# Kernel optimization log

Hardware: AMD Instinct MI355X
Metric: run time of the kernel (lower is better)

Reference implementation:

```python
import jax, jax.numpy as jnp
import numpy as np

B, H, S, DK, DV = 2, 48, 2048, 128, 128
EPS = 1e-6

def _l2norm(x):
    n = jnp.linalg.norm(x, axis=-1, keepdims=True)
    return x / jnp.maximum(n, EPS)

def setup_inputs() -> dict:
    root = jax.random.key(0)
    k0, k1, k2, k3, k4 = jax.random.split(root, 5)
    query = jax.random.normal(k0, (B, H, S, DK), jnp.float32)
    key = jax.random.normal(k1, (B, H, S, DK), jnp.float32)
    value = jax.random.normal(k2, (B, H, S, DV), jnp.float32)
    # g is a per-token log decay: negative, in (-0.5, 0)
    g = -0.5 * jax.random.uniform(k3, (B, H, S), jnp.float32)
    # beta is a sigmoid-like mixing gate in (0, 1)
    beta = jax.random.uniform(k4, (B, H, S), jnp.float32)
    return {"query": query, "key": key, "value": value, "g": g, "beta": beta}

def reference(query, key, value, g, beta):
    """Gated delta-rule linear-attention recurrence.

    state_t = state_{t-1} * exp(g_t)
    delta_t = (v_t - k_t^T state_t) * beta_t
    state_t = state_t + k_t delta_t^T
    out_t   = q_t^T state_t
    with q, k L2-normalized and q scaled by 1/sqrt(dk).
    Returns (output [B,H,S,DV], final_state [B,H,DK,DV]).
    """
    dk = query.shape[-1]
    scale = 1.0 / np.sqrt(dk).astype(np.float32)
    q = _l2norm(query) * scale
    k = _l2norm(key)
    # move seq axis to front for scan: (S, B, H, d)
    qs = jnp.moveaxis(q, 2, 0)
    ks = jnp.moveaxis(k, 2, 0)
    vs = jnp.moveaxis(value, 2, 0)
    gs = jnp.moveaxis(g, 2, 0)
    bs = jnp.moveaxis(beta, 2, 0)

    def step(state, xs):
        q_t, k_t, v_t, g_t, b_t = xs
        state = state * jnp.exp(g_t)[..., None, None]          # [B,H,DK,DV]
        kv_mem = jnp.einsum('bhk,bhkv->bhv', k_t, state)       # read
        delta = (v_t - kv_mem) * b_t[..., None]                # beta-scaled delta
        state = state + jnp.einsum('bhk,bhv->bhkv', k_t, delta)
        out = jnp.einsum('bhk,bhkv->bhv', q_t, state)
        return state, out

    init = jnp.zeros((query.shape[0], query.shape[1], dk, value.shape[-1]), query.dtype)
    final_state, outs = jax.lax.scan(step, init, (qs, ks, vs, gs, bs))
    output = jnp.moveaxis(outs, 0, 2)  # [B,H,S,DV]
    return output, final_state
```

## Files before the change

### kernel.cpp

```cpp
#include <hip/hip_runtime.h>

typedef __attribute__((ext_vector_type(8)))  short short8;
typedef __attribute__((ext_vector_type(4)))  float f32x4;
typedef __attribute__((ext_vector_type(16))) float f32x16;
typedef __attribute__((ext_vector_type(4)))  unsigned short ushort4v;

#define NH   96
#define SEQL 2048
#define DD   128
#define CC   64
#define NCH  32
#define SK   136
#define S64  72
#define SLOT 4608

__device__ __forceinline__ unsigned short f2bf(float f){
  union { float f; unsigned u; } v; v.f = f;
  unsigned r = v.u + 0x7FFFu + ((v.u >> 16) & 1u);
  return (unsigned short)(r >> 16);
}
__device__ __forceinline__ float bf2f(unsigned short u){
  union { unsigned u; float f; } v; v.u = ((unsigned)u) << 16; return v.f;
}
__device__ __forceinline__ short8 frg(const unsigned short* b, int stride, int row0, int kt, int lane){
  return *(const short8*)&b[(row0 + (lane & 31)) * stride + (kt << 4) + ((lane >> 5) << 3)];
}
__device__ __forceinline__ short8 ifrag(int n0, int kt, int lane){
  const int idx = n0 + (lane & 31) - (kt << 4) - ((lane >> 5) << 3);
  short8 v;
  #pragma unroll
  for (int e = 0; e < 8; ++e) v[e] = (short)((e == idx) ? 0x3F80 : 0);
  return v;
}
#define MM32(A,B,C) __builtin_amdgcn_mfma_f32_32x32x16_bf16(A,B,C,0,0,0)
__device__ __forceinline__ f32x16 z16(){
  return (f32x16){0.f,0.f,0.f,0.f,0.f,0.f,0.f,0.f,0.f,0.f,0.f,0.f,0.f,0.f,0.f,0.f};
}
template<int KTN>
__device__ __forceinline__ f32x16 gemm32(const unsigned short* A, int sa, int m0,
                                         const unsigned short* B, int sb, int n0,
                                         f32x16 acc, int lane){
  #pragma unroll
  for (int kt = 0; kt < KTN; ++kt)
    acc = MM32(frg(A, sa, m0, kt, lane), frg(B, sb, n0, kt, lane), acc);
  return acc;
}
__device__ __forceinline__ void stq(unsigned short* buf, int stride, int n0, int m0, int lane, f32x16 v){
  const int nn = n0 + (lane & 31), hh = (lane >> 5) << 2;
  #pragma unroll
  for (int q = 0; q < 4; ++q) {
    ushort4v pv;
    #pragma unroll
    for (int s = 0; s < 4; ++s) pv[s] = f2bf(v[4*q + s]);
    *(ushort4v*)&buf[nn * stride + m0 + 8*q + hh] = pv;
  }
}
__device__ __forceinline__ void stqf(float* buf, int stride, int n0, int m0, int lane, f32x16 v){
  const int nn = n0 + (lane & 31), hh = (lane >> 5) << 2;
  #pragma unroll
  for (int q = 0; q < 4; ++q) {
    f32x4 pv;
    #pragma unroll
    for (int s = 0; s < 4; ++s) pv[s] = v[4*q + s];
    *(f32x4*)&buf[nn * stride + m0 + 8*q + hh] = pv;
  }
}
__device__ __forceinline__ f32x16 ldq(const unsigned short* buf, int stride, int n0, int m0, int lane){
  f32x16 a;
  const int nn = n0 + (lane & 31), hh = (lane >> 5) << 2;
  #pragma unroll
  for (int q = 0; q < 4; ++q) {
    ushort4v pv = *(const ushort4v*)&buf[nn * stride + m0 + 8*q + hh];
    #pragma unroll
    for (int s = 0; s < 4; ++s) a[4*q + s] = bf2f(pv[s]);
  }
  return a;
}
__device__ __forceinline__ f32x16 pinit(const unsigned short* lo, const unsigned short* hi,
                                        int nt, int m0, int lane){
  const unsigned short* base = (nt ? hi : lo) + (lane & 31) * S64;
  const int hh = (lane >> 5) << 2;
  f32x16 p;
  #pragma unroll
  for (int q = 0; q < 4; ++q) {
    ushort4v t = *(const ushort4v*)&base[m0 + 8*q + hh];
    #pragma unroll
    for (int s = 0; s < 4; ++s) p[4*q + s] = bf2f(t[s]);
  }
  return p;
}
#define BAR() do { asm volatile("s_waitcnt lgkmcnt(0)" ::: "memory"); __builtin_amdgcn_s_barrier(); } while(0)

#define REC  36864
#define QOFF 0
#define WOFF 8192
#define UOFF 16384
#define KOFF 24576
#define MOFF 32768

#define AOF 0
#define BOF 9216
#define XS0 17920
#define XS1 22528
#define XS2 27136
#define XS3 31744
#define MRO 36352

__global__ __launch_bounds__(256, 2)
void gdn_prep(const float* __restrict__ Qg, const float* __restrict__ Kg,
              const float* __restrict__ Vg, const float* __restrict__ Gg,
              const float* __restrict__ Bg,
              unsigned short* __restrict__ wsp, float* __restrict__ wcs)
{
  __shared__ unsigned short a[40448];
  __shared__ float s_swv[64], s_swiv[64], s_sbe[64];

  const int tid = threadIdx.x, w = tid >> 6, lane = tid & 63;
  const int mt = w >> 1, nt = w & 1;
  const int hc = blockIdx.x, head = hc >> 5, c = hc & 31;
  const int t0 = c * CC;
  const size_t rb = (size_t)head * SEQL * DD + (size_t)t0 * DD;
  const float* kp = Kg + rb;
  const float* qp = Qg + rb;
  const float* vp = Vg + rb;
  const float* gp = Gg + (size_t)head * SEQL + t0;
  const float* bp = Bg + (size_t)head * SEQL + t0;
  unsigned short* rec = wsp + (size_t)hc * REC;

  const int lrow = tid >> 2, cb = (tid & 3) * 32;
  const int cq16 = (tid & 3) * 16;

  f32x4 kr[8], qr[8], vr[8];
  #pragma unroll
  for (int i = 0; i < 8; ++i) {
    kr[i] = *(const f32x4*)(kp + (size_t)lrow * DD + cb + 4*i);
    qr[i] = *(const f32x4*)(qp + (size_t)lrow * DD + cb + 4*i);
    vr[i] = *(const f32x4*)(vp + (size_t)lrow * DD + cb + 4*i);
  }
  float gl = gp[lane], bl = bp[lane];
  float sc = gl;
  #pragma unroll
  for (int d = 1; d < 64; d <<= 1) { float t = __shfl_up(sc, d); if (lane >= d) sc += t; }
  float wv = __expf(sc);
  if (w == 0) { s_swv[lane] = wv; s_swiv[lane] = __expf(-sc); s_sbe[lane] = bl; }
  float ssk = 0.f, ssq = 0.f;
  #pragma unroll
  for (int i = 0; i < 8; ++i) {
    ssk += kr[i][0]*kr[i][0] + kr[i][1]*kr[i][1] + kr[i][2]*kr[i][2] + kr[i][3]*kr[i][3];
    ssq += qr[i][0]*qr[i][0] + qr[i][1]*qr[i][1] + qr[i][2]*qr[i][2] + qr[i][3]*qr[i][3];
  }
  ssk += __shfl_xor(ssk, 1); ssk += __shfl_xor(ssk, 2);
  ssq += __shfl_xor(ssq, 1); ssq += __shfl_xor(ssq, 2);
  const float ik = 1.f / fmaxf(sqrtf(ssk), 1e-6f);
  const float wl = __shfl(wv, lrow);
  const float iq = 0.08838834764831845f / fmaxf(sqrtf(ssq), 1e-6f) * wl;
  #pragma unroll
  for (int i = 0; i < 8; ++i) {
    ushort4v pk, pq;
    #pragma unroll
    for (int r = 0; r < 4; ++r) { pk[r] = f2bf(kr[i][r]*ik); pq[r] = f2bf(qr[i][r]*iq); }
    *(ushort4v*)&a[AOF + lrow*SK + cb + 4*i] = pk;
    *(ushort4v*)&a[BOF + lrow*SK + cb + 4*i] = pq;
    *(ushort4v*)(rec + QOFF + lrow*DD + cb + 4*i) = pq;
  }
  BAR();

  {
    f32x16 ckk = gemm32<8>(a+AOF, SK, 32*mt, a+AOF, SK, 32*nt, z16(), lane);
    f32x16 ckq = gemm32<8>(a+AOF, SK, 32*mt, a+BOF, SK, 32*nt, z16(), lane);
    const int nn = 32*nt + (lane & 31), hh = (lane >> 5) << 2;
    const float ben = s_sbe[nn], wvn = s_swv[nn], sin = s_swiv[nn];
    #pragma unroll
    for (int q = 0; q < 4; ++q) {
      ushort4v xT, xR, mv;
      #pragma unroll
      for (int si = 0; si < 4; ++si) {
        const int r = 4*q + si, mm = 32*mt + 8*q + hh + si;
        const float svm = s_swv[mm], sim = s_swiv[mm], bem = s_sbe[mm];
        xT[si] = (mm > nn) ? f2bf(bem*svm*sin*ckk[r]) : 0;
        xR[si] = (nn > mm) ? f2bf(ben*wvn*sim*ckk[r]) : 0;
        mv[si] = (mm <= nn) ? f2bf(ckq[r]*sim) : 0;
      }
      const int off = nn*S64 + 32*mt + 8*q + hh;
      *(ushort4v*)&a[XS1 + off] = xT;
      *(ushort4v*)&a[XS0 + off] = xR;
      const int blk = (32*mt + 8*q + hh) >> 2;
      *(ushort4v*)&a[MRO + nn*64 + ((blk ^ (nn & 15)) << 2)] = mv;
    }
  }
  BAR();

  {
    f32x16 c1 = gemm32<4>(a+XS0, S64, 32*mt, a+XS1, S64, 32*nt, z16(), lane);
    f32x16 c2 = gemm32<4>(a+XS1, S64, 32*mt, a+XS0, S64, 32*nt, z16(), lane);
    stq(a+XS3, S64, 32*nt, 32*mt, lane, c1);
    stq(a+XS2, S64, 32*nt, 32*mt, lane, c2);
    unsigned short* p0 = a + ((lrow < 32) ? BOF : BOF+2304) + (lrow & 31)*S64;
    const unsigned short* x0 = a + XS0 + lrow*S64;
    #pragma unroll
    for (int jj = 0; jj < 2; ++jj) {
      short8 xv = *(const short8*)&x0[cq16 + 8*jj];
      short8 ov;
      #pragma unroll
      for (int e = 0; e < 8; ++e) {
        const int col = cq16 + 8*jj + e;
        ov[e] = (short)f2bf(((col == lrow) ? 1.f : 0.f) - bf2f((unsigned short)xv[e]));
      }
      *(short8*)&p0[cq16 + 8*jj] = ov;
    }
    #pragma unroll
    for (int b = 0; b < 4; ++b) {
      const int blk = (cq16 >> 2) + b, bh = blk ^ (lrow & 15);
      unsigned long long v = *(const unsigned long long*)&a[MRO + lrow*64 + bh*4];
      *(unsigned long long*)(rec + MOFF + lrow*64 + cq16 + b*4) = v;
    }
  }
  BAR();

  #pragma unroll
  for (int lev = 0; lev < 2; ++lev) {
    const int sr = (lev & 1) ? XS0 : XS2;
    const int st = (lev & 1) ? XS1 : XS3;
    const int dr = (lev & 1) ? XS2 : XS0;
    const int dt = (lev & 1) ? XS3 : XS1;
    const int pp = lev & 1;
    unsigned short* plo_s = a + (pp ? BOF+SLOT : BOF);
    unsigned short* phi_s = a + (pp ? MRO : BOF+2304);
    unsigned short* plo_d = a + (pp ? BOF : BOF+SLOT);
    unsigned short* phi_d = a + (pp ? BOF+2304 : MRO);
    f32x16 c1 = gemm32<4>(a+sr, S64, 32*mt, a+st, S64, 32*nt, z16(), lane);
    if (lev < 1) {
      f32x16 c2 = gemm32<4>(a+st, S64, 32*mt, a+sr, S64, 32*nt, z16(), lane);
      stq(a+dt, S64, 32*nt, 32*mt, lane, c1);
      stq(a+dr, S64, 32*nt, 32*mt, lane, c2);
    } else {
      stq(a+XS2, S64, 32*nt, 32*mt, lane, c1);
    }
    f32x16 p = pinit(plo_s, phi_s, nt, 32*mt, lane);
    p = gemm32<4>(a+st, S64, 32*mt, (nt ? phi_s : plo_s), S64, 0, p, lane);
    stq((nt ? phi_d : plo_d), S64, 0, 32*mt, lane, p);
    BAR();
  }

  {
    f32x16 p = pinit(a+BOF, a+BOF+2304, nt, 32*mt, lane);
    p = gemm32<4>(a+XS2, S64, 32*mt, (nt ? a+BOF+2304 : a+BOF), S64, 0, p, lane);
    stq((nt ? a+MRO : a+BOF+SLOT), S64, 0, 32*mt, lane, p);
    #pragma unroll
    for (int i = 0; i < 8; ++i)
      #pragma unroll
      for (int r = 0; r < 4; ++r)
        a[XS0 + (cb + 4*i + r)*S64 + lrow] = f2bf(vr[i][r]);
  }
  BAR();

  {
    unsigned short* trow  = a + ((lrow < 32) ? BOF+SLOT : MRO) + (lrow & 31)*S64;
    unsigned short* t3row = a + ((lrow < 32) ? BOF : BOF+2304) + (lrow & 31)*S64;
    #pragma unroll
    for (int jj = 0; jj < 2; ++jj) {
      short8 tv = *(const short8*)&trow[cq16 + 8*jj];
      short8 o2, o3;
      #pragma unroll
      for (int e = 0; e < 8; ++e) {
        const int j = cq16 + 8*jj + e;
        const float t = bf2f((unsigned short)tv[e]);
        o2[e] = (short)f2bf(-t * s_sbe[j] * s_swv[j]);
        o3[e] = (short)f2bf( t * s_sbe[j]);
      }
      *(short8*)&trow[cq16 + 8*jj]  = o2;
      *(short8*)&t3row[cq16 + 8*jj] = o3;
    }
    #pragma unroll
    for (int j = 0; j < 2; ++j) {
      f32x16 ckt = z16();
      #pragma unroll
      for (int kk = 0; kk < 2; ++kk) {
        const int kt = 2*w + kk;
        ckt = MM32(frg(a+AOF, SK, 32*j, kt, lane), ifrag(32*w, kt, lane), ckt);
      }
      stq(a+XS2, S64, 32*w, 32*j, lane, ckt);
    }
  }
  BAR();

  f32x16 uacc[2];
  {
    #pragma unroll
    for (int j = 0; j < 2; ++j) {
      f32x16 cw = gemm32<4>(a+XS2, S64, 32*w, (j ? a+MRO : a+BOF+SLOT), S64, 0, z16(), lane);
      stq(a+AOF, SK, 32*j, 32*w, lane, cw);
      uacc[j] = gemm32<4>((j ? a+BOF+2304 : a+BOF), S64, 0, a+XS0, S64, 32*w, z16(), lane);
    }
  }
  BAR();

  {
    const int r2 = tid >> 2, seg = (tid & 3) * 32;
    #pragma unroll
    for (int j2 = 0; j2 < 4; ++j2) {
      short8 v8 = *(const short8*)&a[AOF + r2*SK + seg + 8*j2];
      *(short8*)(rec + WOFF + r2*128 + seg + 8*j2) = v8;
    }
    const int r = tid >> 1, half = (tid & 1) * 32;
    const float wc = s_swv[63];
    #pragma unroll
    for (int j2 = 0; j2 < 4; ++j2) {
      short8 kv = *(const short8*)&a[XS2 + r*S64 + half + 8*j2];
      short8 o;
      #pragma unroll
      for (int e = 0; e < 8; ++e) {
        const int tok = half + 8*j2 + e;
        o[e] = (short)f2bf(bf2f((unsigned short)kv[e]) * wc * s_swiv[tok]);
      }
      *(short8*)(rec + KOFF + r*64 + half + 8*j2) = o;
    }
    unsigned short* uq = a + ((w == 0) ? BOF : (w == 1) ? BOF+2304 : (w == 2) ? BOF+SLOT : MRO);
    stq(uq, S64, 0, 0, lane, uacc[0]);
    stq(uq, S64, 0, 32, lane, uacc[1]);
    if (tid == 0) wcs[hc] = wc;
  }
  BAR();

  {
    const int r = tid >> 1, half = (tid & 1) * 32;
    const unsigned short* qb = a + ((r < 32) ? BOF : (r < 64) ? BOF+2304 : (r < 96) ? BOF+SLOT : MRO);
    #pragma unroll
    for (int j2 = 0; j2 < 4; ++j2) {
      short8 v8 = *(const short8*)&qb[(r & 31)*S64 + half + 8*j2];
      *(short8*)(rec + UOFF + r*64 + half + 8*j2) = v8;
    }
  }
}

#define SU   72
#define OW   0
#define OK0  8704
#define OK1  17920
#define OU   27136
#define OM0  31744
#define OM1  36352
#define OS0T 40960
#define ODT  49664

__global__ __launch_bounds__(512, 1)
void gdn_scan(const unsigned short* __restrict__ wsp, const float* __restrict__ wcs,
              float* __restrict__ Out, float* __restrict__ FS)
{
  __shared__ unsigned short a[54272];
  __shared__ float s_ob[64*68];

  const int tid = threadIdx.x, w = tid >> 6, lane = tid & 63;
  const int head = blockIdx.x % NH, vh = blockIdx.x / NH;
  const unsigned short* recs = wsp + (size_t)head * NCH * REC;
  float* op = Out + (size_t)head * SEQL * DD + vh * 64;

  const int mtS = w >> 1, ntS = w & 1;
  const int mt4 = (w & 3) >> 1, nt4 = w & 1;

  f32x16 s = z16(), oqr = z16();

  const int wr = tid >> 3, wc16 = (tid & 7) * 16;
  const int kr = tid >> 2, kc16 = (tid & 3) * 16;
  const int ur = tid >> 3, uc8 = (tid & 7) * 8;

  short8 stW0, stW1, stK0, stK1, stU, stM, qb[8];
  float wc_cur = 0.f, wcn = 0.f;

  auto issue = [&](int c){
    const unsigned short* rec = recs + (size_t)c * REC;
    stW0 = *(const short8*)(rec + WOFF + wr*128 + wc16);
    stW1 = *(const short8*)(rec + WOFF + wr*128 + wc16 + 8);
    stK0 = *(const short8*)(rec + KOFF + kr*64 + kc16);
    stK1 = *(const short8*)(rec + KOFF + kr*64 + kc16 + 8);
    stU  = *(const short8*)(rec + UOFF + (vh*64 + ur)*64 + uc8);
    stM  = *(const short8*)(rec + MOFF + ur*64 + uc8);
    if (w >= 4) {
      #pragma unroll
      for (int kt = 0; kt < 8; ++kt)
        qb[kt] = *(const short8*)(rec + QOFF + (32*nt4 + (lane & 31))*DD + kt*16 + ((lane >> 5) << 3));
    }
    wcn = wcs[head*NCH + c];
  };
  auto dswrite = [&](int par){
    *(short8*)&a[OW + wr*SK + wc16]     = stW0;
    *(short8*)&a[OW + wr*SK + wc16 + 8] = stW1;
    unsigned short* bk = a + (par ? OK1 : OK0);
    *(short8*)&bk[kr*SU + kc16]     = stK0;
    *(short8*)&bk[kr*SU + kc16 + 8] = stK1;
    *(short8*)&a[OU + ur*SU + uc8] = stU;
    unsigned short* bm = a + (par ? OM1 : OM0);
    *(short8*)&bm[ur*SU + uc8] = stM;
  };

  issue(0);
  wc_cur = wcn;
  dswrite(0);
  stq(a+OS0T, SK, 32*ntS, 32*mtS, lane, s);
  BAR();

  for (int c = 0; c < NCH; ++c) {
    const int cur = c & 1;

    if (c > 0) {
      const int row = tid >> 3, c8 = (tid & 7) * 8;
      f32x4 v0 = *(const f32x4*)&s_ob[row*68 + c8];
      f32x4 v1 = *(const f32x4*)&s_ob[row*68 + c8 + 4];
      float* dst = op + (size_t)((c-1)*CC + row) * DD + c8;
      *(f32x4*)dst = v0;
      *(f32x4*)(dst + 4) = v1;
    }
    if (w < 4) {
      f32x16 d = gemm32<8>(a+OW, SK, 32*mt4, a+OS0T, SK, 32*nt4, z16(), lane);
      const int nn = 32*nt4 + (lane & 31), hh = (lane >> 5) << 2;
      #pragma unroll
      for (int q = 0; q < 4; ++q) {
        ushort4v u4 = *(const ushort4v*)&a[OU + nn*SU + 32*mt4 + 8*q + hh];
        ushort4v pt;
        #pragma unroll
        for (int si = 0; si < 4; ++si) pt[si] = f2bf(d[4*q+si] + bf2f(u4[si]));
        *(ushort4v*)&a[ODT + nn*SU + 32*mt4 + 8*q + hh] = pt;
      }
    } else {
      f32x16 o = z16();
      #pragma unroll
      for (int kt = 0; kt < 8; ++kt)
        o = MM32(frg(a+OS0T, SK, 32*mt4, kt, lane), qb[kt], o);
      oqr = o;
    }
    if (c < NCH-1) issue(c+1);
    BAR();

    {
      f32x16 sa;
      #pragma unroll
      for (int r = 0; r < 16; ++r) sa[r] = s[r] * wc_cur;
      s = gemm32<4>(a + (cur ? OK1 : OK0), SU, 32*mtS, a+ODT, SU, 32*ntS, sa, lane);
    }
    if (w >= 4) {
      f32x16 o = gemm32<4>(a+ODT, SU, 32*mt4, a + (cur ? OM1 : OM0), SU, 32*nt4, oqr, lane);
      stqf(s_ob, 68, 32*nt4, 32*mt4, lane, o);
    }
    stq(a+OS0T, SK, 32*ntS, 32*mtS, lane, s);
    if (c < NCH-1) { dswrite(cur ^ 1); wc_cur = wcn; }
    BAR();
  }

  {
    const int row = tid >> 3, c8 = (tid & 7) * 8;
    f32x4 v0 = *(const f32x4*)&s_ob[row*68 + c8];
    f32x4 v1 = *(const f32x4*)&s_ob[row*68 + c8 + 4];
    float* dst = op + (size_t)((NCH-1)*CC + row) * DD + c8;
    *(f32x4*)dst = v0;
    *(f32x4*)(dst + 4) = v1;
  }
  {
    float* fsp = FS + (size_t)head * DD * DD + vh * 64;
    const int nn = 32*ntS + (lane & 31), hh = (lane >> 5) << 2;
    #pragma unroll
    for (int q = 0; q < 4; ++q)
      #pragma unroll
      for (int si = 0; si < 4; ++si)
        fsp[(size_t)(32*mtS + 8*q + hh + si) * DD + nn] = s[4*q + si];
  }
}

__global__ __launch_bounds__(512, 1)
void gdn_chunk2(const float* __restrict__ Qg, const float* __restrict__ Kg,
                const float* __restrict__ Vg, const float* __restrict__ Gg,
                const float* __restrict__ Bg,
                float* __restrict__ Out, float* __restrict__ FS)
{
  __shared__ __align__(16) unsigned short sKc[64*SK];
  __shared__ __align__(16) unsigned short sQc[64*SK];
  __shared__ __align__(16) unsigned short sS0T[64*SK];
  __shared__ __align__(16) unsigned short sVc[64*S64];
  __shared__ __align__(16) unsigned short sVT[64*S64];
  __shared__ __align__(16) unsigned short sM[64*S64];
  __shared__ __align__(16) unsigned short sAr[8*SLOT];
  __shared__ float sbe2[2][64], swv2[2][64], swiv2[2][64];

  const int tid  = threadIdx.x;
  const int w    = tid >> 6;
  const int lane = tid & 63;
  const int half = w >> 2;
  const int j    = w & 3;
  const int mt   = j >> 1, nt = j & 1;
  const int mtS  = w >> 1, ntS = w & 1;
  const int mtK  = w >> 2, ntK = w & 3;
  const int head = blockIdx.x % NH;
  const int vh   = blockIdx.x / NH;

  const size_t rb = (size_t)head * SEQL * DD;
  const float* qp = Qg + rb;
  const float* kp = Kg + rb;
  const float* vp = Vg + rb + vh * 64;
  const float* gp = Gg + (size_t)head * SEQL;
  const float* bp = Bg + (size_t)head * SEQL;
  float* op  = Out + rb + vh * 64;
  float* fsp = FS + (size_t)head * DD * DD + vh * 64;

  const int lrow = tid >> 3;
  const int c16  = (tid & 7) * 16;
  const int c8   = (tid & 7) * 8;

  unsigned short* const sl0 = sAr + 0*SLOT;
  unsigned short* const sl1 = sAr + 1*SLOT;
  unsigned short* const sl2 = sAr + 2*SLOT;
  unsigned short* const sl3 = sAr + 3*SLOT;
  unsigned short* const sl4 = sAr + 4*SLOT;
  unsigned short* const sl5 = sAr + 5*SLOT;
  unsigned short* const sl6 = sAr + 6*SLOT;
  unsigned short* const sl7 = sAr + 7*SLOT;

  f32x16 s = z16(), oacc = z16();
  f32x4 kr[4], qr[4], vr[2]; float gr = 0.f, br = 0.f;

  auto prefetch = [&](int t0p){
    const float* kb = kp + (size_t)(t0p + lrow) * DD + c16;
    const float* qb = qp + (size_t)(t0p + lrow) * DD + c16;
    const float* vb = vp + (size_t)(t0p + lrow) * DD + c8;
    #pragma unroll
    for (int i = 0; i < 4; ++i) { kr[i] = *(const f32x4*)(kb + 4*i); qr[i] = *(const f32x4*)(qb + 4*i); }
    #pragma unroll
    for (int i = 0; i < 2; ++i) vr[i] = *(const f32x4*)(vb + 4*i);
    if (w == 7) { gr = gp[t0p + lane]; br = bp[t0p + lane]; }
  };
  auto scan_to = [&](int p){
    if (w == 7) {
      float sc = gr;
      #pragma unroll
      for (int d = 1; d < 64; d <<= 1) { float t = __shfl_up(sc, d); if (lane >= d) sc += t; }
      swv2[p][lane]  = __expf(sc);
      swiv2[p][lane] = __expf(-sc);
      sbe2[p][lane]  = br;
    }
  };

  prefetch(0);
  scan_to(0);
  BAR();

  for (int tc = 0; tc < NCH; ++tc) {
    const int t0 = tc * CC;
    const int cur = tc & 1, nxt = cur ^ 1;
    {
      float ssk = 0.f, ssq = 0.f;
      #pragma unroll
      for (int i = 0; i < 4; ++i) {
        ssk += kr[i][0]*kr[i][0] + kr[i][1]*kr[i][1] + kr[i][2]*kr[i][2] + kr[i][3]*kr[i][3];
        ssq += qr[i][0]*qr[i][0] + qr[i][1]*qr[i][1] + qr[i][2]*qr[i][2] + qr[i][3]*qr[i][3];
      }
      ssk += __shfl_xor(ssk, 1); ssk += __shfl_xor(ssk, 2); ssk += __shfl_xor(ssk, 4);
      ssq += __shfl_xor(ssq, 1); ssq += __shfl_xor(ssq, 2); ssq += __shfl_xor(ssq, 4);
      const float ik = 1.f / fmaxf(sqrtf(ssk), 1e-6f);
      const float iq = 0.08838834764831845f / fmaxf(sqrtf(ssq), 1e-6f) * swv2[cur][lrow];
      #pragma unroll
      for (int i = 0; i < 4; ++i) {
        ushort4v pk, pq;
        #pragma unroll
        for (int r = 0; r < 4; ++r) { pk[r] = f2bf(kr[i][r] * ik); pq[r] = f2bf(qr[i][r] * iq); }
        *(ushort4v*)&sKc[lrow*SK + c16 + 4*i] = pk;
        *(ushort4v*)&sQc[lrow*SK + c16 + 4*i] = pq;
      }
      #pragma unroll
      for (int i = 0; i < 2; ++i) {
        ushort4v pv;
        #pragma unroll
        for (int r = 0; r < 4; ++r) pv[r] = f2bf(vr[i][r]);
        *(ushort4v*)&sVc[lrow*S64 + c8 + 4*i] = pv;
      }
    }
    stq(sS0T, SK, 32*ntS, 32*mtS, lane, s);
    prefetch(tc < NCH-1 ? (tc+1)*CC : t0);
    BAR();

    if (half == 0) {
      f32x16 aa = gemm32<8>(sKc, SK, 32*mt, sKc, SK, 32*nt, z16(), lane);
      const int nn = 32*nt + (lane & 31), hh = (lane >> 5) << 2;
      #pragma unroll
      for (int q = 0; q < 4; ++q) {
        ushort4v pR, pL, pPT, pP;
        #pragma unroll
        for (int si = 0; si < 4; ++si) {
          const int r = 4*q + si, mm = 32*mt + 8*q + hh + si;
          const float S = aa[r];
          const float av  = (mm > nn) ? sbe2[cur][mm]*swv2[cur][mm]*swiv2[cur][nn]*S : 0.f;
          const float atr = (nn > mm) ? sbe2[cur][nn]*swv2[cur][nn]*swiv2[cur][mm]*S : 0.f;
          pR[si]  = f2bf(av);
          pL[si]  = f2bf(atr);
          pPT[si] = f2bf(((mm==nn)?1.f:0.f) - av);
          pP[si]  = f2bf(((mm==nn)?1.f:0.f) - atr);
        }
        const int off = nn*S64 + 32*mt + 8*q + hh;
        *(ushort4v*)&sl1[off] = pR;
        *(ushort4v*)&sl0[off] = pL;
        *(ushort4v*)&sl5[off] = pPT;
        *(ushort4v*)&sl4[off] = pP;
      }
    } else {
      f32x16 aa = gemm32<8>(sKc, SK, 32*mt, sQc, SK, 32*nt, z16(), lane);
      const int nn = 32*nt + (lane & 31), hh = (lane >> 5) << 2;
      #pragma unroll
      for (int q = 0; q < 4; ++q) {
        ushort4v pv;
        #pragma unroll
        for (int si = 0; si < 4; ++si) {
          const int r = 4*q + si, mm = 32*mt + 8*q + hh + si;
          pv[si] = f2bf((mm <= nn) ? aa[r]*swiv2[cur][mm] : 0.f);
        }
        *(ushort4v*)&sM[nn*S64 + 32*mt + 8*q + hh] = pv;
      }
    }
    BAR();

    if (half == 0) {
      f32x16 aa = gemm32<4>(sl0, S64, 32*mt, sl1, S64, 32*nt, z16(), lane);
      stq(sl3, S64, 32*nt, 32*mt, lane, aa);
      f32x16 bb = z16();
      #pragma unroll
      for (int kk = 0; kk < 2; ++kk) {
        const int kt = 2*nt + kk;
        bb = MM32(frg(sVc, S64, 32*mt, kt, lane), ifrag(32*nt, kt, lane), bb);
      }
      stq(sVT, S64, 32*nt, 32*mt, lane, bb);
    } else {
      f32x16 aa = gemm32<4>(sl1, S64, 32*mt, sl0, S64, 32*nt, z16(), lane);
      stq(sl2, S64, 32*nt, 32*mt, lane, aa);
      oacc = gemm32<8>(sQc, SK, 32*mt, sS0T, SK, 32*nt, z16(), lane);
    }
    BAR();

    {
      unsigned short* const inL[3]   = { sl2, sl0, sl2 };
      unsigned short* const inR[3]   = { sl3, sl1, sl3 };
      unsigned short* const outL[3]  = { sl0, sl2, sl0 };
      unsigned short* const outR[3]  = { sl1, sl3, sl1 };
      unsigned short* const inP[3]   = { sl4, sl7, sl5 };
      unsigned short* const inPT[3]  = { sl5, sl6, sl4 };
      unsigned short* const outP[3]  = { sl7, sl5, sl7 };
      unsigned short* const outPT[3] = { sl6, sl4, sl6 };
      #pragma unroll
      for (int lev = 0; lev < 3; ++lev) {
        if (half == 0) {
          f32x16 aa = gemm32<4>(inL[lev], S64, 32*mt, inR[lev], S64, 32*nt, z16(), lane);
          stq(outR[lev], S64, 32*nt, 32*mt, lane, aa);
          f32x16 p = ldq(inPT[lev], S64, 32*nt, 32*mt, lane);
          p = gemm32<4>(inP[lev], S64, 32*mt, inR[lev], S64, 32*nt, p, lane);
          stq(outPT[lev], S64, 32*nt, 32*mt, lane, p);
        } else {
          f32x16 aa = gemm32<4>(inR[lev], S64, 32*mt, inL[lev], S64, 32*nt, z16(), lane);
          stq(outL[lev], S64, 32*nt, 32*mt, lane, aa);
          f32x16 p = ldq(inP[lev], S64, 32*nt, 32*mt, lane);
          p = gemm32<4>(inR[lev], S64, 32*mt, inP[lev], S64, 32*nt, p, lane);
          stq(outP[lev], S64, 32*nt, 32*mt, lane, p);
        }
        BAR();
      }
    }

    if (half == 0) {
      f32x16 aa = gemm32<4>(sl0, S64, 32*mt, sl1, S64, 32*nt, z16(), lane);
      stq(sl2, S64, 32*nt, 32*mt, lane, aa);
    } else {
      f32x16 p = ldq(sl7, S64, 32*nt, 32*mt, lane);
      p = gemm32<4>(sl1, S64, 32*mt, sl7, S64, 32*nt, p, lane);
      stq(sl4, S64, 32*nt, 32*mt, lane, p);
    }
    BAR();

    if (half == 0) {
      f32x16 p = ldq(sl4, S64, 32*nt, 32*mt, lane);
      p = gemm32<4>(sl2, S64, 32*mt, sl4, S64, 32*nt, p, lane);
      const int nn = 32*nt + (lane & 31), hh = (lane >> 5) << 2;
      #pragma unroll
      for (int q = 0; q < 4; ++q) {
        ushort4v p2, p3;
        #pragma unroll
        for (int si = 0; si < 4; ++si) {
          const int r = 4*q + si, mm = 32*mt + 8*q + hh + si;
          const float t = p[r];
          p2[si] = f2bf(-t * sbe2[cur][mm] * swv2[cur][mm]);
          p3[si] = f2bf( t * sbe2[cur][mm]);
        }
        const int off = nn*S64 + 32*mt + 8*q + hh;
        *(ushort4v*)&sl1[off] = p2;
        *(ushort4v*)&sl5[off] = p3;
      }
    } else {
      f32x16 zz = gemm32<8>(sKc, SK, 32*mt, sS0T, SK, 32*nt, z16(), lane);
      stq(sl0, S64, 32*nt, 32*mt, lane, zz);
    }
    {
      f32x16 aa = z16();
      #pragma unroll
      for (int kk = 0; kk < 2; ++kk) {
        const int kt = 2*ntK + kk;
        aa = MM32(frg(sKc, SK, 32*mtK, kt, lane), ifrag(32*ntK, kt, lane), aa);
      }
      stq(sl6, S64, 32*ntK, 32*mtK, lane, aa);
    }
    BAR();

    if (half == 0) {
      f32x16 d = gemm32<4>(sl5, S64, 32*mt, sVT, S64, 32*nt, z16(), lane);
      d = gemm32<4>(sl1, S64, 32*mt, sl0, S64, 32*nt, d, lane);
      const int nn = 32*nt + (lane & 31), hh = (lane >> 5) << 2;
      const float w63 = swv2[cur][63];
      #pragma unroll
      for (int q = 0; q < 4; ++q) {
        ushort4v pt, ps;
        #pragma unroll
        for (int si = 0; si < 4; ++si) {
          const int r = 4*q + si, mm = 32*mt + 8*q + hh + si;
          pt[si] = f2bf(d[r]);
          ps[si] = f2bf(d[r] * w63 * swiv2[cur][mm]);
        }
        const int off = nn*S64 + 32*mt + 8*q + hh;
        *(ushort4v*)&sl3[off] = pt;
        *(ushort4v*)&sl2[off] = ps;
      }
    }
    scan_to(nxt);
    {
      const float w63 = swv2[cur][63];
      #pragma unroll
      for (int r = 0; r < 16; ++r) s[r] *= w63;
    }
    BAR();

    s = gemm32<4>(sl6, S64, 32*mtS, sl2, S64, 32*ntS, s, lane);
    if (half == 1) {
      f32x16 o = oacc;
      o = gemm32<4>(sM, S64, 32*mt, sl3, S64, 32*nt, o, lane);
      const int nn = 32*nt + (lane & 31), hh = (lane >> 5) << 2;
      #pragma unroll
      for (int q = 0; q < 4; ++q)
        #pragma unroll
        for (int si = 0; si < 4; ++si)
          op[(size_t)(t0 + 32*mt + 8*q + hh + si) * DD + nn] = o[4*q + si];
    }
    BAR();
  }

  {
    const int nn = 32*ntS + (lane & 31), hh = (lane >> 5) << 2;
    #pragma unroll
    for (int q = 0; q < 4; ++q)
      #pragma unroll
      for (int si = 0; si < 4; ++si)
        fsp[(size_t)(32*mtS + 8*q + hh + si) * DD + nn] = s[4*q + si];
  }
}

extern "C" void kernel_launch(void* const* d_in, const int* in_sizes, int n_in,
                              void* d_out, int out_size, void* d_ws, size_t ws_size,
                              hipStream_t stream) {
  const float* Q = (const float*)d_in[0];
  const float* K = (const float*)d_in[1];
  const float* V = (const float*)d_in[2];
  const float* G = (const float*)d_in[3];
  const float* B = (const float*)d_in[4];
  float* Out = (float*)d_out;
  float* FS  = Out + (size_t)NH * SEQL * DD;

  const size_t WS_NEED = (size_t)NH * NCH * REC * 2 + (size_t)NH * NCH * 4;
  if (ws_size >= WS_NEED) {
    unsigned short* wsp = (unsigned short*)d_ws;
    float* wcs = (float*)(wsp + (size_t)NH * NCH * REC);
    hipLaunchKernelGGL(gdn_prep, dim3(NH*NCH), dim3(256), 0, stream, Q, K, V, G, B, wsp, wcs);
    hipLaunchKernelGGL(gdn_scan, dim3(NH*2), dim3(512), 0, stream, wsp, wcs, Out, FS);
  } else {
    hipLaunchKernelGGL(gdn_chunk2, dim3(NH*2), dim3(512), 0, stream, Q, K, V, G, B, Out, FS);
  }
}
```

Baseline: 254.8 us.

## Double-buffer scan state and operands to drop one barrier per chunk

The scan loop now double-buffers the W, U and state tiles in LDS. All eight waves compute the delta-term product redundantly instead of splitting it, so the mid-chunk barrier is removed and each chunk needs only one barrier. Output is written straight from registers to global memory rather than staged through an LDS buffer. The precompute kernel also writes W, U, M and K records directly from registers, removing an extra LDS staging pass and two barriers. In exchange LDS use and redundant MFMA work per chunk go up, and the direct global output stores are strided.

```diff
diff --git a/kernel.cpp b/kernel.cpp
--- a/kernel.cpp
+++ b/kernel.cpp
@@ -53,16 +53,6 @@
     #pragma unroll
     for (int s = 0; s < 4; ++s) pv[s] = f2bf(v[4*q + s]);
     *(ushort4v*)&buf[nn * stride + m0 + 8*q + hh] = pv;
-  }
-}
-__device__ __forceinline__ void stqf(float* buf, int stride, int n0, int m0, int lane, f32x16 v){
-  const int nn = n0 + (lane & 31), hh = (lane >> 5) << 2;
-  #pragma unroll
-  for (int q = 0; q < 4; ++q) {
-    f32x4 pv;
-    #pragma unroll
-    for (int s = 0; s < 4; ++s) pv[s] = v[4*q + s];
-    *(f32x4*)&buf[nn * stride + m0 + 8*q + hh] = pv;
   }
 }
 __device__ __forceinline__ f32x16 ldq(const unsigned short* buf, int stride, int n0, int m0, int lane){
@@ -184,8 +174,7 @@
       const int off = nn*S64 + 32*mt + 8*q + hh;
       *(ushort4v*)&a[XS1 + off] = xT;
       *(ushort4v*)&a[XS0 + off] = xR;
-      const int blk = (32*mt + 8*q + hh) >> 2;
-      *(ushort4v*)&a[MRO + nn*64 + ((blk ^ (nn & 15)) << 2)] = mv;
+      *(ushort4v*)(rec + MOFF + nn*64 + 32*mt + 8*q + hh) = mv;
     }
   }
   BAR();
@@ -207,12 +196,6 @@
         ov[e] = (short)f2bf(((col == lrow) ? 1.f : 0.f) - bf2f((unsigned short)xv[e]));
       }
       *(short8*)&p0[cq16 + 8*jj] = ov;
-    }
-    #pragma unroll
-    for (int b = 0; b < 4; ++b) {
-      const int blk = (cq16 >> 2) + b, bh = blk ^ (lrow & 15);
-      unsigned long long v = *(const unsigned long long*)&a[MRO + lrow*64 + bh*4];
-      *(unsigned long long*)(rec + MOFF + lrow*64 + cq16 + b*4) = v;
     }
   }
   BAR();
@@ -271,6 +254,7 @@
       *(short8*)&trow[cq16 + 8*jj]  = o2;
       *(short8*)&t3row[cq16 + 8*jj] = o3;
     }
+    const float wcv = s_swv[63];
     #pragma unroll
     for (int j = 0; j < 2; ++j) {
       f32x16 ckt = z16();
@@ -280,92 +264,82 @@
         ckt = MM32(frg(a+AOF, SK, 32*j, kt, lane), ifrag(32*w, kt, lane), ckt);
       }
       stq(a+XS2, S64, 32*w, 32*j, lane, ckt);
+      const int nn = 32*w + (lane & 31), hh = (lane >> 5) << 2;
+      #pragma unroll
+      for (int q = 0; q < 4; ++q) {
+        ushort4v o;
+        #pragma unroll
+        for (int si = 0; si < 4; ++si) {
+          const int tok = 32*j + 8*q + hh + si;
+          o[si] = f2bf(ckt[4*q+si] * wcv * s_swiv[tok]);
+        }
+        *(ushort4v*)(rec + KOFF + nn*64 + 32*j + 8*q + hh) = o;
+      }
     }
   }
   BAR();
 
-  f32x16 uacc[2];
   {
+    const int nn = lane & 31, hh = (lane >> 5) << 2;
     #pragma unroll
     for (int j = 0; j < 2; ++j) {
       f32x16 cw = gemm32<4>(a+XS2, S64, 32*w, (j ? a+MRO : a+BOF+SLOT), S64, 0, z16(), lane);
-      stq(a+AOF, SK, 32*j, 32*w, lane, cw);
-      uacc[j] = gemm32<4>((j ? a+BOF+2304 : a+BOF), S64, 0, a+XS0, S64, 32*w, z16(), lane);
-    }
-  }
-  BAR();
-
-  {
-    const int r2 = tid >> 2, seg = (tid & 3) * 32;
-    #pragma unroll
-    for (int j2 = 0; j2 < 4; ++j2) {
-      short8 v8 = *(const short8*)&a[AOF + r2*SK + seg + 8*j2];
-      *(short8*)(rec + WOFF + r2*128 + seg + 8*j2) = v8;
-    }
-    const int r = tid >> 1, half = (tid & 1) * 32;
-    const float wc = s_swv[63];
-    #pragma unroll
-    for (int j2 = 0; j2 < 4; ++j2) {
-      short8 kv = *(const short8*)&a[XS2 + r*S64 + half + 8*j2];
-      short8 o;
-      #pragma unroll
-      for (int e = 0; e < 8; ++e) {
-        const int tok = half + 8*j2 + e;
-        o[e] = (short)f2bf(bf2f((unsigned short)kv[e]) * wc * s_swiv[tok]);
-      }
-      *(short8*)(rec + KOFF + r*64 + half + 8*j2) = o;
-    }
-    unsigned short* uq = a + ((w == 0) ? BOF : (w == 1) ? BOF+2304 : (w == 2) ? BOF+SLOT : MRO);
-    stq(uq, S64, 0, 0, lane, uacc[0]);
-    stq(uq, S64, 0, 32, lane, uacc[1]);
-    if (tid == 0) wcs[hc] = wc;
-  }
-  BAR();
-
-  {
-    const int r = tid >> 1, half = (tid & 1) * 32;
-    const unsigned short* qb = a + ((r < 32) ? BOF : (r < 64) ? BOF+2304 : (r < 96) ? BOF+SLOT : MRO);
-    #pragma unroll
-    for (int j2 = 0; j2 < 4; ++j2) {
-      short8 v8 = *(const short8*)&qb[(r & 31)*S64 + half + 8*j2];
-      *(short8*)(rec + UOFF + r*64 + half + 8*j2) = v8;
-    }
+      #pragma unroll
+      for (int q = 0; q < 4; ++q) {
+        ushort4v pw;
+        #pragma unroll
+        for (int si = 0; si < 4; ++si) pw[si] = f2bf(cw[4*q+si]);
+        *(ushort4v*)(rec + WOFF + (32*j + nn)*128 + 32*w + 8*q + hh) = pw;
+      }
+      f32x16 cu = gemm32<4>((j ? a+BOF+2304 : a+BOF), S64, 0, a+XS0, S64, 32*w, z16(), lane);
+      #pragma unroll
+      for (int q = 0; q < 4; ++q) {
+        ushort4v pu;
+        #pragma unroll
+        for (int si = 0; si < 4; ++si) pu[si] = f2bf(cu[4*q+si]);
+        *(ushort4v*)(rec + UOFF + (32*w + nn)*64 + 32*j + 8*q + hh) = pu;
+      }
+    }
+    if (tid == 0) wcs[hc] = s_swv[63];
   }
 }
 
 #define SU   72
-#define OW   0
-#define OK0  8704
-#define OK1  17920
-#define OU   27136
-#define OM0  31744
-#define OM1  36352
-#define OS0T 40960
-#define ODT  49664
+#define OW0  0
+#define OW1  8704
+#define OK0  17408
+#define OK1  26624
+#define OU0  35840
+#define OU1  40448
+#define OM0  45056
+#define OM1  49664
+#define OS0  54272
+#define OS1  62976
+#define ODT  71680
 
 __global__ __launch_bounds__(512, 1)
 void gdn_scan(const unsigned short* __restrict__ wsp, const float* __restrict__ wcs,
               float* __restrict__ Out, float* __restrict__ FS)
 {
-  __shared__ unsigned short a[54272];
-  __shared__ float s_ob[64*68];
+  __shared__ unsigned short a[76288];
 
   const int tid = threadIdx.x, w = tid >> 6, lane = tid & 63;
   const int head = blockIdx.x % NH, vh = blockIdx.x / NH;
   const unsigned short* recs = wsp + (size_t)head * NCH * REC;
+  const float* wcsh = wcs + head * NCH;
   float* op = Out + (size_t)head * SEQL * DD + vh * 64;
 
   const int mtS = w >> 1, ntS = w & 1;
-  const int mt4 = (w & 3) >> 1, nt4 = w & 1;
-
-  f32x16 s = z16(), oqr = z16();
+  const bool outw = (w < 4);
+
+  f32x16 s = z16();
 
   const int wr = tid >> 3, wc16 = (tid & 7) * 16;
   const int kr = tid >> 2, kc16 = (tid & 3) * 16;
   const int ur = tid >> 3, uc8 = (tid & 7) * 8;
 
   short8 stW0, stW1, stK0, stK1, stU, stM, qb[8];
-  float wc_cur = 0.f, wcn = 0.f;
+  float wcn = 0.f;
 
   auto issue = [&](int c){
     const unsigned short* rec = recs + (size_t)c * REC;
@@ -375,85 +349,92 @@
     stK1 = *(const short8*)(rec + KOFF + kr*64 + kc16 + 8);
     stU  = *(const short8*)(rec + UOFF + (vh*64 + ur)*64 + uc8);
     stM  = *(const short8*)(rec + MOFF + ur*64 + uc8);
-    if (w >= 4) {
+    if (outw) {
       #pragma unroll
       for (int kt = 0; kt < 8; ++kt)
-        qb[kt] = *(const short8*)(rec + QOFF + (32*nt4 + (lane & 31))*DD + kt*16 + ((lane >> 5) << 3));
-    }
-    wcn = wcs[head*NCH + c];
+        qb[kt] = *(const short8*)(rec + QOFF + (32*mtS + (lane & 31))*DD + kt*16 + ((lane >> 5) << 3));
+    }
+    wcn = wcsh[c];
   };
   auto dswrite = [&](int par){
-    *(short8*)&a[OW + wr*SK + wc16]     = stW0;
-    *(short8*)&a[OW + wr*SK + wc16 + 8] = stW1;
+    unsigned short* bw = a + (par ? OW1 : OW0);
+    *(short8*)&bw[wr*SK + wc16]     = stW0;
+    *(short8*)&bw[wr*SK + wc16 + 8] = stW1;
     unsigned short* bk = a + (par ? OK1 : OK0);
     *(short8*)&bk[kr*SU + kc16]     = stK0;
     *(short8*)&bk[kr*SU + kc16 + 8] = stK1;
-    *(short8*)&a[OU + ur*SU + uc8] = stU;
+    unsigned short* bu = a + (par ? OU1 : OU0);
+    *(short8*)&bu[ur*SU + uc8] = stU;
     unsigned short* bm = a + (par ? OM1 : OM0);
     *(short8*)&bm[ur*SU + uc8] = stM;
   };
 
   issue(0);
-  wc_cur = wcn;
+  float wc_cur = wcn;
   dswrite(0);
-  stq(a+OS0T, SK, 32*ntS, 32*mtS, lane, s);
+  stq(a+OS0, SK, 32*ntS, 32*mtS, lane, s);
   BAR();
 
   for (int c = 0; c < NCH; ++c) {
     const int cur = c & 1;
-
-    if (c > 0) {
-      const int row = tid >> 3, c8 = (tid & 7) * 8;
-      f32x4 v0 = *(const f32x4*)&s_ob[row*68 + c8];
-      f32x4 v1 = *(const f32x4*)&s_ob[row*68 + c8 + 4];
-      float* dst = op + (size_t)((c-1)*CC + row) * DD + c8;
-      *(f32x4*)dst = v0;
-      *(f32x4*)(dst + 4) = v1;
-    }
-    if (w < 4) {
-      f32x16 d = gemm32<8>(a+OW, SK, 32*mt4, a+OS0T, SK, 32*nt4, z16(), lane);
-      const int nn = 32*nt4 + (lane & 31), hh = (lane >> 5) << 2;
+    const unsigned short* W_ = a + (cur ? OW1 : OW0);
+    const unsigned short* K_ = a + (cur ? OK1 : OK0);
+    const unsigned short* U_ = a + (cur ? OU1 : OU0);
+    const unsigned short* M_ = a + (cur ? OM1 : OM0);
+    const unsigned short* S_ = a + (cur ? OS1 : OS0);
+    unsigned short* Sn       = a + (cur ? OS0 : OS1);
+
+    f32x16 oq = z16();
+    if (outw) {
+      #pragma unroll
+      for (int kt = 0; kt < 8; ++kt)
+        oq = MM32(qb[kt], frg(S_, SK, 32*ntS, kt, lane), oq);
+    }
+    if (c < NCH-1) issue(c+1);
+
+    {
+      f32x16 d0 = gemm32<8>(W_, SK, 0,  S_, SK, 32*ntS, z16(), lane);
+      f32x16 d1 = gemm32<8>(W_, SK, 32, S_, SK, 32*ntS, z16(), lane);
+      const int nn = 32*ntS + (lane & 31), hh = (lane >> 5) << 2;
       #pragma unroll
       for (int q = 0; q < 4; ++q) {
-        ushort4v u4 = *(const ushort4v*)&a[OU + nn*SU + 32*mt4 + 8*q + hh];
-        ushort4v pt;
-        #pragma unroll
-        for (int si = 0; si < 4; ++si) pt[si] = f2bf(d[4*q+si] + bf2f(u4[si]));
-        *(ushort4v*)&a[ODT + nn*SU + 32*mt4 + 8*q + hh] = pt;
-      }
-    } else {
-      f32x16 o = z16();
-      #pragma unroll
-      for (int kt = 0; kt < 8; ++kt)
-        o = MM32(frg(a+OS0T, SK, 32*mt4, kt, lane), qb[kt], o);
-      oqr = o;
-    }
-    if (c < NCH-1) issue(c+1);
-    BAR();
+        ushort4v u0 = *(const ushort4v*)&U_[nn*SU + 0  + 8*q + hh];
+        ushort4v u1 = *(const ushort4v*)&U_[nn*SU + 32 + 8*q + hh];
+        ushort4v p0, p1;
+        #pragma unroll
+        for (int si = 0; si < 4; ++si) {
+          p0[si] = f2bf(d0[4*q+si] + bf2f(u0[si]));
+          p1[si] = f2bf(d1[4*q+si] + bf2f(u1[si]));
+        }
+        *(ushort4v*)&a[ODT + nn*SU + 0  + 8*q + hh] = p0;
+        *(ushort4v*)&a[ODT + nn*SU + 32 + 8*q + hh] = p1;
+      }
+    }
 
     {
       f32x16 sa;
       #pragma unroll
       for (int r = 0; r < 16; ++r) sa[r] = s[r] * wc_cur;
-      s = gemm32<4>(a + (cur ? OK1 : OK0), SU, 32*mtS, a+ODT, SU, 32*ntS, sa, lane);
-    }
-    if (w >= 4) {
-      f32x16 o = gemm32<4>(a+ODT, SU, 32*mt4, a + (cur ? OM1 : OM0), SU, 32*nt4, oqr, lane);
-      stqf(s_ob, 68, 32*nt4, 32*mt4, lane, o);
-    }
-    stq(a+OS0T, SK, 32*ntS, 32*mtS, lane, s);
-    if (c < NCH-1) { dswrite(cur ^ 1); wc_cur = wcn; }
-    BAR();
-  }
-
-  {
-    const int row = tid >> 3, c8 = (tid & 7) * 8;
-    f32x4 v0 = *(const f32x4*)&s_ob[row*68 + c8];
-    f32x4 v1 = *(const f32x4*)&s_ob[row*68 + c8 + 4];
-    float* dst = op + (size_t)((NCH-1)*CC + row) * DD + c8;
-    *(f32x4*)dst = v0;
-    *(f32x4*)(dst + 4) = v1;
-  }
+      s = gemm32<4>(K_, SU, 32*mtS, a+ODT, SU, 32*ntS, sa, lane);
+    }
+
+    if (outw) {
+      f32x16 o = gemm32<4>(M_, SU, 32*mtS, a+ODT, SU, 32*ntS, oq, lane);
+      const int vv = 32*ntS + (lane & 31), hh = (lane >> 5) << 2;
+      float* ob = op + (size_t)(c*CC + 32*mtS) * DD + vv;
+      #pragma unroll
+      for (int q = 0; q < 4; ++q)
+        #pragma unroll
+        for (int si = 0; si < 4; ++si)
+          ob[(size_t)(si + 8*q + hh) * DD] = o[4*q + si];
+    }
+
+    stq(Sn, SK, 32*ntS, 32*mtS, lane, s);
+    if (c < NCH-1) dswrite(cur ^ 1);
+    wc_cur = wcn;
+    BAR();
+  }
+
   {
     float* fsp = FS + (size_t)head * DD * DD + vh * 64;
     const int nn = 32*ntS + (lane & 31), hh = (lane >> 5) << 2;
@@ -461,7 +442,7 @@
     for (int q = 0; q < 4; ++q)
       #pragma unroll
       for (int si = 0; si < 4; ++si)
-        fsp[(size_t)(32*mtS + 8*q + hh + si) * DD + nn] = s[4*q + si];
+        fsp[(size_t)(32*mtS + si + 8*q + hh) * DD + nn] = s[4*q + si];
   }
 }
 
```

New measurement: 257.7 us. No clear change (+1.1%).
